# Performance work log

Hardware: AMD Instinct MI355X
Metric: run time of the kernel (lower is better)

## Reference

```python
import jax, jax.numpy as jnp
import numpy as np

N, E = 2048, 32768
IN_ND, ND = 128, 256
IN_ED, ED = 64, 128
OUT_D = 256
H, FF, NL = 8, 1024, 3
MAX_DEG = 64
L = 5


def setup_inputs() -> dict:
    key = jax.random.key(0)
    ks = jax.random.split(key, 20)
    s = 0.02
    return dict(
        x=jax.random.normal(ks[0], (N, IN_ND), jnp.float32),
        edge_index=jax.random.randint(ks[1], (2, E), 0, N),
        edge_attr=jax.random.normal(ks[2], (E, IN_ED), jnp.float32),
        node_dist=jax.random.randint(ks[3], (N, N), 0, 7, dtype=jnp.int32),
        edge_paths=jax.random.randint(ks[4], (N, N, L), 0, E, dtype=jnp.int32),
        Wn_in=jax.random.normal(ks[5], (IN_ND, ND)) * s,
        bn_in=jnp.zeros((ND,)),
        We_in=jax.random.normal(ks[6], (IN_ED, ED)) * s,
        be_in=jnp.zeros((ED,)),
        z_in=jax.random.normal(ks[7], (MAX_DEG, ND)) * s,
        z_out=jax.random.normal(ks[8], (MAX_DEG, ND)) * s,
        b_spatial=jax.random.normal(ks[9], (L,)) * s,
        ln1_w=jnp.ones((NL, ND)), ln1_b=jnp.zeros((NL, ND)),
        ln2_w=jnp.ones((NL, ND)), ln2_b=jnp.zeros((NL, ND)),
        Wq=jax.random.normal(ks[10], (NL, H, ND, ND)) * s,
        bq=jnp.zeros((NL, H, ND)),
        Wk=jax.random.normal(ks[11], (NL, H, ND, ND)) * s,
        bk=jnp.zeros((NL, H, ND)),
        Wv=jax.random.normal(ks[12], (NL, H, ND, ND)) * s,
        bv=jnp.zeros((NL, H, ND)),
        edge_vec=jax.random.normal(ks[13], (NL, H, L, ED)) * s,
        Wo=jax.random.normal(ks[14], (NL, H * ND, ND)) * s,
        bo=jnp.zeros((NL, ND)),
        Wff1=jax.random.normal(ks[15], (NL, ND, FF)) * s,
        bff1=jnp.zeros((NL, FF)),
        Wff2=jax.random.normal(ks[16], (NL, FF, ND)) * s,
        bff2=jnp.zeros((NL, ND)),
        Wout=jax.random.normal(ks[17], (ND, OUT_D)) * s,
        bout=jnp.zeros((OUT_D,)),
    )


def _ln(x, w, b, eps=1e-5):
    m = x.mean(-1, keepdims=True)
    v = ((x - m) ** 2).mean(-1, keepdims=True)
    return (x - m) * jax.lax.rsqrt(v + eps) * w + b


def _forward(x, edge_attr, Wn_in, bn_in, We_in, be_in, z_in, z_out, b_spatial,
             ln1_w, ln1_b, ln2_w, ln2_b, Wq, bq, Wk, bk, Wv, bv, edge_vec,
             Wo, bo, Wff1, bff1, Wff2, bff2, Wout, bout,
             edge_index, node_dist, edge_paths):
    n = x.shape[0]
    h = x @ Wn_in + bn_in                      # node_in_lin
    e = edge_attr @ We_in + be_in              # edge_in_lin
    # centrality encoding: degree embeddings, clipped to table size - 1
    in_deg = jnp.zeros((n,), jnp.int32).at[edge_index[1]].add(1)
    out_deg = jnp.zeros((n,), jnp.int32).at[edge_index[0]].add(1)
    h = h + z_in[jnp.clip(in_deg, 0, z_in.shape[0] - 1)] \
          + z_out[jnp.clip(out_deg, 0, z_out.shape[0] - 1)]
    # spatial encoding: b[min(path_len, L) - 1], 0 where unreachable
    Lmax = b_spatial.shape[0]
    b_mat = jnp.where(node_dist > 0,
                      b_spatial[jnp.clip(node_dist, 1, Lmax) - 1],
                      jnp.zeros((), h.dtype))          # [N,N]
    n_pe = jnp.clip(node_dist - 1, 0, Lmax)            # edges on path
    inv_len = jnp.where(n_pe > 0,
                        1.0 / jnp.maximum(n_pe, 1).astype(h.dtype),
                        jnp.zeros((), h.dtype))        # [N,N]
    nl, nh, _, dk = Wq.shape
    scale = 1.0 / jnp.sqrt(jnp.asarray(dk, h.dtype))
    for l in range(nl):
        xn = _ln(h, ln1_w[l], ln1_b[l])
        q = jnp.einsum('nd,hdk->hnk', xn, Wq[l]) + bq[l][:, None, :]
        k = jnp.einsum('nd,hdk->hnk', xn, Wk[l]) + bk[l][:, None, :]
        v = jnp.einsum('nd,hdk->hnk', xn, Wv[l]) + bv[l][:, None, :]
        # edge encoding: per-head dot of edge_vector[step] with each edge feature,
        # then gather along the stored shortest path and mean over its length
        dots = jnp.einsum('hld,ed->hle', edge_vec[l], e)   # [H,L,E]
        c = jnp.zeros((nh, n, n), h.dtype)
        for s in range(Lmax):  # fixed small loop over path steps
            d_s = jnp.take(dots[:, s, :], edge_paths[:, :, s], axis=1)  # [H,N,N]
            valid = (s < n_pe)[None]                                    # [1,N,N]
            c = c + jnp.where(valid, d_s, jnp.zeros((), h.dtype))
        c = c * inv_len[None]
        a = jnp.einsum('hnk,hmk->hnm', q, k) * scale + b_mat[None] + c
        attn = jax.nn.softmax(a, axis=-1)
        o = jnp.einsum('hnm,hmk->hnk', attn, v)            # [H,N,dk]
        o = jnp.transpose(o, (1, 0, 2)).reshape(n, nh * dk)
        h = o @ Wo[l] + bo[l] + h                          # attn + residual
        x2 = _ln(h, ln2_w[l], ln2_b[l])
        h = jax.nn.gelu(x2 @ Wff1[l] + bff1[l], approximate=False) @ Wff2[l] + bff2[l] + h
    return h @ Wout + bout


def reference(x, edge_index, edge_attr, node_dist, edge_paths,
              Wn_in, bn_in, We_in, be_in, z_in, z_out, b_spatial,
              ln1_w, ln1_b, ln2_w, ln2_b, Wq, bq, Wk, bk, Wv, bv, edge_vec,
              Wo, bo, Wff1, bff1, Wff2, bff2, Wout, bout):
    return _forward(x, edge_attr, Wn_in, bn_in, We_in, be_in, z_in, z_out,
                    b_spatial, ln1_w, ln1_b, ln2_w, ln2_b, Wq, bq, Wk, bk,
                    Wv, bv, edge_vec, Wo, bo, Wff1, bff1, Wff2, bff2,
                    Wout, bout, edge_index, node_dist, edge_paths)
```

## Files before the change

kernel.cpp:

```cpp
#include <hip/hip_runtime.h>


constexpr int NN    = 2048;
constexpr int EE    = 32768;
constexpr int IN_ND = 128;
constexpr int ND    = 256;
constexpr int IN_ED = 64;
constexpr int ED    = 128;
constexpr int H     = 8;
constexpr int FF    = 1024;
constexpr int NL    = 3;
constexpr int LMAX  = 5;
constexpr int MAXDEG= 64;
constexpr int SPLIT = 4;
constexpr int KSP   = NN / SPLIT;
constexpr int QROWS = 256;

enum { E_NONE = 0, E_BIAS = 1, E_BIAS_RES = 2, E_BIAS_GELU = 3 };

using u16 = unsigned short;
using short8 = __attribute__((ext_vector_type(8))) short;
using f32x4  = __attribute__((ext_vector_type(4))) float;
using u32x4  = __attribute__((ext_vector_type(4))) unsigned int;

__device__ __forceinline__ u16 f2bf(float f) {
    unsigned u = __float_as_uint(f);
    u += 0x7fff + ((u >> 16) & 1);
    return (u16)(u >> 16);
}
__device__ __forceinline__ float bf2f(u16 h) {
    return __uint_as_float((unsigned)h << 16);
}
__device__ __forceinline__ float gelu_f(float x) {
    return 0.5f * x * (1.0f + erff(x * 0.70710678118654752440f));
}

#define GLL16(gsrc, ldst)                                                     \
    __builtin_amdgcn_global_load_lds(                                         \
        (const __attribute__((address_space(1))) void*)(gsrc),                \
        (__attribute__((address_space(3))) void*)(ldst), 16, 0, 0)

template<int EPI, int OBF>
__global__ __launch_bounds__(256)
void mgemm_k(const u16* __restrict__ A, int lda, long aZs,
             const u16* __restrict__ B, int ldb, long bZs,
             void* __restrict__ Cp, int ldc, long cZs,
             int K, const float* __restrict__ bias0,
             const float* __restrict__ bias1, const float* __restrict__ bias2)
{
    const int z = blockIdx.z;
    A += (long)z * aZs;
    B += (long)z * bZs;
    const float* bias = (z == 0) ? bias0 : (z == 1 ? bias1 : bias2);
    const int row0 = blockIdx.y * 128, col0 = blockIdx.x * 128;
    const int tid = threadIdx.x;
    const int lane = tid & 63, wv = tid >> 6;
    const int wr = wv >> 1, wc = wv & 1;
    const int fl = lane & 15, kg = lane >> 4;

    __shared__ u16 As[128 * 32];
    __shared__ u16 Bs[128 * 32];

    int aoff[4], boff[4];
#pragma unroll
    for (int m = 0; m < 4; m++) {
        int r = wr * 64 + m * 16 + fl;
        aoff[m] = r * 64 + ((kg ^ ((r >> 1) & 3)) * 16);
        r = wc * 64 + m * 16 + fl;
        boff[m] = r * 64 + ((kg ^ ((r >> 1) & 3)) * 16);
    }

    const int id0 = tid * 2, id1 = id0 + 1;
    const int sr0 = id0 >> 2, sl0 = id0 & 3;
    const int sr1 = id1 >> 2, sl1 = id1 & 3;
    const int wb0 = sr0 * 64 + ((sl0 ^ ((sr0 >> 1) & 3)) * 16);
    const int wb1 = sr1 * 64 + ((sl1 ^ ((sr1 >> 1) & 3)) * 16);
    const u16* ga0 = A + (long)(row0 + sr0) * lda + sl0 * 8;
    const u16* ga1 = A + (long)(row0 + sr1) * lda + sl1 * 8;
    const u16* gb0 = B + (long)(col0 + sr0) * ldb + sl0 * 8;
    const u16* gb1 = B + (long)(col0 + sr1) * ldb + sl1 * 8;

    const f32x4 zero = {0.f, 0.f, 0.f, 0.f};
    f32x4 acc[4][4];
#pragma unroll
    for (int m = 0; m < 4; m++)
#pragma unroll
        for (int n = 0; n < 4; n++) acc[m][n] = zero;

    for (int k0 = 0; k0 < K; k0 += 32) {
        const uint4 va0 = *(const uint4*)(ga0 + k0);
        const uint4 va1 = *(const uint4*)(ga1 + k0);
        const uint4 vb0 = *(const uint4*)(gb0 + k0);
        const uint4 vb1 = *(const uint4*)(gb1 + k0);
        __syncthreads();
        *(uint4*)((char*)As + wb0) = va0;
        *(uint4*)((char*)As + wb1) = va1;
        *(uint4*)((char*)Bs + wb0) = vb0;
        *(uint4*)((char*)Bs + wb1) = vb1;
        __syncthreads();
        short8 af[4], bfr[4];
#pragma unroll
        for (int m = 0; m < 4; m++)
            af[m] = *(const short8*)((const char*)As + aoff[m]);
#pragma unroll
        for (int n = 0; n < 4; n++)
            bfr[n] = *(const short8*)((const char*)Bs + boff[n]);
#pragma unroll
        for (int m = 0; m < 4; m++)
#pragma unroll
            for (int n = 0; n < 4; n++)
                acc[m][n] = __builtin_amdgcn_mfma_f32_16x16x32_bf16(
                    af[m], bfr[n], acc[m][n], 0, 0, 0);
    }

    float* Cf = (float*)Cp + (long)z * cZs;
    u16*   Cb = (u16*)Cp   + (long)z * cZs;
#pragma unroll
    for (int n = 0; n < 4; n++) {
        const int col = col0 + wc * 64 + n * 16 + fl;
        float bcol = 0.f;
        if constexpr (EPI == E_BIAS || EPI == E_BIAS_RES || EPI == E_BIAS_GELU)
            bcol = bias[col];
#pragma unroll
        for (int m = 0; m < 4; m++) {
            const f32x4 v = acc[m][n];
#pragma unroll
            for (int r = 0; r < 4; r++) {
                const int row = row0 + wr * 64 + m * 16 + kg * 4 + r;
                float x = v[r];
                if constexpr (EPI == E_BIAS)       x += bcol;
                else if constexpr (EPI == E_BIAS_RES)  x += bcol + Cf[(long)row * ldc + col];
                else if constexpr (EPI == E_BIAS_GELU) x = gelu_f(x + bcol);
                if constexpr (OBF) Cb[(long)row * ldc + col] = f2bf(x);
                else               Cf[(long)row * ldc + col] = x;
            }
        }
    }
}

template<int EPI, int OBF>
__global__ __launch_bounds__(256)
void mgemm64_k(const u16* __restrict__ A, int lda,
               const u16* __restrict__ B, int ldb,
               void* __restrict__ Cp, int ldc,
               int K, const float* __restrict__ bias)
{
    const int row0 = blockIdx.y * 64, col0 = blockIdx.x * 64;
    const int tid = threadIdx.x, lane = tid & 63, w = tid >> 6;
    const int wr = w >> 1, wc = w & 1;
    const int fl = lane & 15, kg = lane >> 4;

    __shared__ u16 As[64 * 64];
    __shared__ u16 Bs[64 * 64];

    int aoff[2][2], boff[2][2];
#pragma unroll
    for (int m = 0; m < 2; m++)
#pragma unroll
        for (int ks = 0; ks < 2; ks++) {
            int r = wr * 32 + m * 16 + fl;
            aoff[m][ks] = r * 64 + (((ks * 4 + kg) ^ (r & 7)) * 8);
            r = wc * 32 + m * 16 + fl;
            boff[m][ks] = r * 64 + (((ks * 4 + kg) ^ (r & 7)) * 8);
        }
    const int i0 = tid, i1 = tid + 256;
    const int ar0 = i0 >> 3, as0 = i0 & 7, ar1 = i1 >> 3, as1 = i1 & 7;
    const u16* gA0 = A + (long)(row0 + ar0) * lda + ((as0 ^ (ar0 & 7)) * 8);
    const u16* gA1 = A + (long)(row0 + ar1) * lda + ((as1 ^ (ar1 & 7)) * 8);
    const u16* gB0 = B + (long)(col0 + ar0) * ldb + ((as0 ^ (ar0 & 7)) * 8);
    const u16* gB1 = B + (long)(col0 + ar1) * ldb + ((as1 ^ (ar1 & 7)) * 8);

    const f32x4 zero = {0.f, 0.f, 0.f, 0.f};
    f32x4 acc[2][2];
#pragma unroll
    for (int m = 0; m < 2; m++)
#pragma unroll
        for (int n = 0; n < 2; n++) acc[m][n] = zero;

    for (int k0 = 0; k0 < K; k0 += 64) {
        const uint4 a0 = *(const uint4*)(gA0 + k0);
        const uint4 a1 = *(const uint4*)(gA1 + k0);
        const uint4 b0 = *(const uint4*)(gB0 + k0);
        const uint4 b1 = *(const uint4*)(gB1 + k0);
        __syncthreads();
        *(uint4*)((char*)As + i0 * 16) = a0;
        *(uint4*)((char*)As + i1 * 16) = a1;
        *(uint4*)((char*)Bs + i0 * 16) = b0;
        *(uint4*)((char*)Bs + i1 * 16) = b1;
        __syncthreads();
        short8 af[2][2], bf_[2][2];
#pragma unroll
        for (int m = 0; m < 2; m++)
#pragma unroll
            for (int ks = 0; ks < 2; ks++) {
                af[m][ks]  = *(const short8*)(As + aoff[m][ks]);
                bf_[m][ks] = *(const short8*)(Bs + boff[m][ks]);
            }
#pragma unroll
        for (int m = 0; m < 2; m++)
#pragma unroll
            for (int n = 0; n < 2; n++)
#pragma unroll
                for (int ks = 0; ks < 2; ks++)
                    acc[m][n] = __builtin_amdgcn_mfma_f32_16x16x32_bf16(
                        af[m][ks], bf_[n][ks], acc[m][n], 0, 0, 0);
    }

    float* Cf = (float*)Cp;
    u16*   Cb = (u16*)Cp;
#pragma unroll
    for (int n = 0; n < 2; n++) {
        const int col = col0 + wc * 32 + n * 16 + fl;
        float bcol = 0.f;
        if constexpr (EPI == E_BIAS || EPI == E_BIAS_RES || EPI == E_BIAS_GELU)
            bcol = bias[col];
#pragma unroll
        for (int m = 0; m < 2; m++) {
            const f32x4 v = acc[m][n];
#pragma unroll
            for (int r = 0; r < 4; r++) {
                const int row = row0 + wr * 32 + m * 16 + kg * 4 + r;
                float x = v[r];
                if constexpr (EPI == E_BIAS)       x += bcol;
                else if constexpr (EPI == E_BIAS_RES)  x += bcol + Cf[(long)row * ldc + col];
                else if constexpr (EPI == E_BIAS_GELU) x = gelu_f(x + bcol);
                if constexpr (OBF) Cb[(long)row * ldc + col] = f2bf(x);
                else               Cf[(long)row * ldc + col] = x;
            }
        }
    }
}

__global__ __launch_bounds__(1024, 4)
void fattn_k(const u16* __restrict__ qb, const u16* __restrict__ kb,
             const u16* __restrict__ vT, u16* __restrict__ sc,
             float* __restrict__ ml)
{
    const int hh = blockIdx.x;
    const int row0 = blockIdx.y * QROWS;
    const int sp = blockIdx.z;
    const int kbase = sp * KSP;
    constexpr int NT = KSP / 32;
    const int tid = threadIdx.x, lane = tid & 63, w = tid >> 6;
    const int fl = lane & 15, kg = lane >> 4;
    const long NN2 = (long)NN * NN;

    __shared__ u16 Ks[3 * 32 * 256];
    __shared__ u16 Vs[3 * 256 * 32];
    __shared__ u16 Bls[2 * 256 * 32];
    __shared__ u16 Ps[16 * 16 * 40];

    auto stage = [&](int t, int buf) {
        const int kt0 = kbase + t * 32;
        const int kr = tid >> 5, ksl = tid & 31;
        GLL16(kb + (long)(kt0 + kr) * (H * ND) + hh * ND + ((ksl ^ (kr & 7)) * 8),
              Ks + buf * 8192 + tid * 8);
        const int vr = tid >> 2, vsl = tid & 3;
        GLL16(vT + (long)(hh * ND + vr) * NN + kt0 + ((vsl ^ ((vr >> 1) & 3)) * 8),
              Vs + buf * 8192 + tid * 8);
    };
    auto stage_bias = [&](int t, int buf) {
        const u16* g = sc + (long)hh * NN2 + (long)(row0 + (tid >> 2)) * NN
                     + kbase + t * 32 + (tid & 3) * 8;
        GLL16(g, Bls + buf * 8192 + tid * 8);
    };

    short8 qf[8];
    {
        const u16* qrow = qb + (long)(row0 + w * 16 + fl) * (H * ND) + hh * ND;
#pragma unroll
        for (int ks = 0; ks < 8; ks++)
            qf[ks] = *(const short8*)(qrow + ks * 32 + kg * 8);
    }
    stage_bias(0, 0);
    stage(0, 0);
    stage(1, 1);

    short8 ones;
#pragma unroll
    for (int i = 0; i < 8; i++) ones[i] = (short)0x3F80;

    f32x4 O[16];
#pragma unroll
    for (int of = 0; of < 16; of++) O[of] = f32x4{0.f, 0.f, 0.f, 0.f};
    f32x4 lac = {0.f, 0.f, 0.f, 0.f};

    const float scale = 1.f / 16.f;
    for (int t = 0; t < NT; t++) {
        asm volatile("s_waitcnt vmcnt(2)" ::: "memory");
        __builtin_amdgcn_sched_barrier(0);
        asm volatile("s_barrier" ::: "memory");
        __builtin_amdgcn_sched_barrier(0);

        stage_bias((t + 1) % NT, (t + 1) & 1);
        stage((t + 2) % NT, (t + 2) % 3);

        const int cb = t % 3;
        f32x4 s[2] = {f32x4{0.f,0.f,0.f,0.f}, f32x4{0.f,0.f,0.f,0.f}};
        __builtin_amdgcn_s_setprio(1);
#pragma unroll
        for (int ks = 0; ks < 8; ks++)
#pragma unroll
            for (int cf = 0; cf < 2; cf++) {
                const int mlr = cf * 16 + fl;
                const short8 kf = *(const short8*)(Ks + cb * 8192 + mlr * 256
                                                   + (((ks * 4 + kg) ^ (mlr & 7)) * 8));
                s[cf] = __builtin_amdgcn_mfma_f32_16x16x32_bf16(qf[ks], kf, s[cf], 0, 0, 0);
            }
        __builtin_amdgcn_s_setprio(0);

        const u16* bl = Bls + (t & 1) * 8192 + (w * 16 + kg * 4) * 32;
        float p[2][4];
#pragma unroll
        for (int cf = 0; cf < 2; cf++)
#pragma unroll
            for (int r = 0; r < 4; r++)
                p[cf][r] = __expf(s[cf][r] * scale
                                  + bf2f(bl[r * 32 + cf * 16 + fl]));
#pragma unroll
        for (int cf = 0; cf < 2; cf++)
#pragma unroll
            for (int r = 0; r < 4; r++)
                Ps[w * 640 + (kg * 4 + r) * 40 + cf * 16 + fl] = f2bf(p[cf][r]);

        const short8 pa = *(const short8*)(Ps + w * 640 + fl * 40 + kg * 8);
        __builtin_amdgcn_s_setprio(1);
        lac = __builtin_amdgcn_mfma_f32_16x16x32_bf16(pa, ones, lac, 0, 0, 0);
#pragma unroll
        for (int of = 0; of < 16; of++) {
            const int d = of * 16 + fl;
            const short8 vf = *(const short8*)(Vs + cb * 8192 + d * 32
                                               + ((kg ^ ((d >> 1) & 3)) * 8));
            O[of] = __builtin_amdgcn_mfma_f32_16x16x32_bf16(pa, vf, O[of], 0, 0, 0);
        }
        __builtin_amdgcn_s_setprio(0);
    }

    u16* op = sc + (long)hh * NN2 + sp * KSP;
#pragma unroll
    for (int of = 0; of < 16; of++)
#pragma unroll
        for (int r = 0; r < 4; r++) {
            const int row = row0 + w * 16 + kg * 4 + r;
            op[(long)row * NN + of * 16 + fl] = f2bf(O[of][r]);
        }
    if (fl == 0) {
#pragma unroll
        for (int r = 0; r < 4; r++) {
            const int row = row0 + w * 16 + kg * 4 + r;
            ml[((long)sp * H + hh) * NN + row] = lac[r];
        }
    }
}

__global__ __launch_bounds__(256)
void combine_k(const u16* __restrict__ sc, const float* __restrict__ ml,
               u16* __restrict__ o2)
{
    const int idx = blockIdx.x * 256 + threadIdx.x;
    const int d8 = idx & 31;
    const int n  = (idx >> 5) & (NN - 1);
    const int h  = idx >> 16;
    const long NN2 = (long)NN * NN;
    float L = 0.f;
#pragma unroll
    for (int z = 0; z < SPLIT; z++)
        L += ml[((long)z * H + h) * NN + n];
    const float invL = 1.f / L;
    float acc[8] = {0.f,0.f,0.f,0.f,0.f,0.f,0.f,0.f};
#pragma unroll
    for (int z = 0; z < SPLIT; z++) {
        const u32x4 q = *(const u32x4*)(sc + (long)h * NN2 + (long)n * NN
                                        + z * KSP + d8 * 8);
        acc[0] += bf2f(q.x & 0xffff); acc[1] += bf2f(q.x >> 16);
        acc[2] += bf2f(q.y & 0xffff); acc[3] += bf2f(q.y >> 16);
        acc[4] += bf2f(q.z & 0xffff); acc[5] += bf2f(q.z >> 16);
        acc[6] += bf2f(q.w & 0xffff); acc[7] += bf2f(q.w >> 16);
    }
    uint4 o;
    o.x = (unsigned)f2bf(acc[0] * invL) | ((unsigned)f2bf(acc[1] * invL) << 16);
    o.y = (unsigned)f2bf(acc[2] * invL) | ((unsigned)f2bf(acc[3] * invL) << 16);
    o.z = (unsigned)f2bf(acc[4] * invL) | ((unsigned)f2bf(acc[5] * invL) << 16);
    o.w = (unsigned)f2bf(acc[6] * invL) | ((unsigned)f2bf(acc[7] * invL) << 16);
    *(uint4*)(o2 + (long)n * (H * ND) + h * ND + d8 * 8) = o;
}

template<int INF32>
__global__ __launch_bounds__(256)
void transp_k(const void* __restrict__ inp, long inZs,
              u16* __restrict__ out, long outZs, int R, int C)
{
    const int z = blockIdx.z;
    const int r0 = blockIdx.y * 64, c0 = blockIdx.x * 64;
    __shared__ u16 t[64][68];
    const int tx = threadIdx.x & 63, ty = threadIdx.x >> 6;
    if constexpr (INF32) {
        const float* in = (const float*)inp + (long)z * inZs;
#pragma unroll
        for (int i = 0; i < 16; i++) {
            const int r = i * 4 + ty;
            t[r][tx] = f2bf(in[(long)(r0 + r) * C + c0 + tx]);
        }
    } else {
        const u16* in = (const u16*)inp + (long)z * inZs;
#pragma unroll
        for (int i = 0; i < 16; i++) {
            const int r = i * 4 + ty;
            t[r][tx] = in[(long)(r0 + r) * C + c0 + tx];
        }
    }
    __syncthreads();
    u16* o = out + (long)z * outZs;
#pragma unroll
    for (int i = 0; i < 16; i++) {
        const int r = i * 4 + ty;
        o[(long)(c0 + r) * R + r0 + tx] = t[tx][r];
    }
}

__global__ __launch_bounds__(256)
void cvt_k(const float* __restrict__ in, u16* __restrict__ out)
{
    const long i = (long)blockIdx.x * 256 + threadIdx.x;
    const float4 v = ((const float4*)in)[i];
    ushort4 o;
    o.x = f2bf(v.x); o.y = f2bf(v.y); o.z = f2bf(v.z); o.w = f2bf(v.w);
    ((ushort4*)out)[i] = o;
}

__global__ __launch_bounds__(256)
void ln_k(const float* __restrict__ x, const float* __restrict__ w,
          const float* __restrict__ b, u16* __restrict__ y)
{
    const int wid = threadIdx.x >> 6, lane = threadIdx.x & 63;
    const int row = blockIdx.x * 4 + wid;
    const float4 v = reinterpret_cast<const float4*>(x + (long)row * ND)[lane];
    float s = v.x + v.y + v.z + v.w;
#pragma unroll
    for (int o = 32; o >= 1; o >>= 1) s += __shfl_xor(s, o);
    const float mean = s * (1.f / ND);
    const float d0 = v.x - mean, d1 = v.y - mean, d2 = v.z - mean, d3 = v.w - mean;
    float sq = d0 * d0 + d1 * d1 + d2 * d2 + d3 * d3;
#pragma unroll
    for (int o = 32; o >= 1; o >>= 1) sq += __shfl_xor(sq, o);
    const float rstd = rsqrtf(sq * (1.f / ND) + 1e-5f);
    const float4 wv = reinterpret_cast<const float4*>(w)[lane];
    const float4 bv = reinterpret_cast<const float4*>(b)[lane];
    ushort4 o4;
    o4.x = f2bf(d0 * rstd * wv.x + bv.x);
    o4.y = f2bf(d1 * rstd * wv.y + bv.y);
    o4.z = f2bf(d2 * rstd * wv.z + bv.z);
    o4.w = f2bf(d3 * rstd * wv.w + bv.w);
    reinterpret_cast<ushort4*>(y + (long)row * ND)[lane] = o4;
}

__global__ __launch_bounds__(256)
void dotsT_k(const u16* __restrict__ e, const float* __restrict__ evl,
             u16* __restrict__ dtb)
{
    const int s = blockIdx.y;
    const int ei = blockIdx.x * 256 + threadIdx.x;
    __shared__ float evs[H * ED];
    for (int i = threadIdx.x; i < H * ED; i += 256)
        evs[i] = evl[((i >> 7) * LMAX + s) * ED + (i & 127)];
    __syncthreads();
    const uint4* er = (const uint4*)(e + (long)ei * ED);
    float c[H];
#pragma unroll
    for (int h = 0; h < H; h++) c[h] = 0.f;
#pragma unroll
    for (int d8 = 0; d8 < ED / 8; d8++) {
        const uint4 q = er[d8];
        float f[8];
        f[0] = bf2f(q.x & 0xffff); f[1] = bf2f(q.x >> 16);
        f[2] = bf2f(q.y & 0xffff); f[3] = bf2f(q.y >> 16);
        f[4] = bf2f(q.z & 0xffff); f[5] = bf2f(q.z >> 16);
        f[6] = bf2f(q.w & 0xffff); f[7] = bf2f(q.w >> 16);
#pragma unroll
        for (int h = 0; h < H; h++) {
            const float* w = &evs[h * ED + d8 * 8];
            c[h] += w[0] * f[0] + w[1] * f[1] + w[2] * f[2] + w[3] * f[3]
                  + w[4] * f[4] + w[5] * f[5] + w[6] * f[6] + w[7] * f[7];
        }
    }
    uint4 o;
    o.x = (unsigned)f2bf(c[0]) | ((unsigned)f2bf(c[1]) << 16);
    o.y = (unsigned)f2bf(c[2]) | ((unsigned)f2bf(c[3]) << 16);
    o.z = (unsigned)f2bf(c[4]) | ((unsigned)f2bf(c[5]) << 16);
    o.w = (unsigned)f2bf(c[6]) | ((unsigned)f2bf(c[7]) << 16);
    *(uint4*)(dtb + ((long)s * EE + ei) * H) = o;
}

__global__ __launch_bounds__(256)
void pack_k(const int* __restrict__ ndist, const int* __restrict__ epaths,
            unsigned* __restrict__ pc0, unsigned* __restrict__ pc1,
            unsigned* __restrict__ pc2)
{
    const long idx = (long)blockIdx.x * 256 + threadIdx.x;
    const unsigned d = (unsigned)ndist[idx];
    const int* ep = epaths + idx * LMAX;
    const unsigned e0 = ep[0], e1 = ep[1], e2 = ep[2], e3 = ep[3], e4 = ep[4];
    pc0[idx] = d | (e0 << 8);
    pc1[idx] = e1 | (e2 << 16);
    pc2[idx] = e3 | (e4 << 16);
}

__global__ __launch_bounds__(256)
void bias_k(const unsigned* __restrict__ pc0, const unsigned* __restrict__ pc1,
            const unsigned* __restrict__ pc2, const float* __restrict__ bspat,
            const u16* __restrict__ dtb, u16* __restrict__ sc)
{
    const long idx = (long)blockIdx.x * 256 + threadIdx.x;
    const unsigned w0 = pc0[idx], w1 = pc1[idx], w2 = pc2[idx];
    const int d = (int)(w0 & 255u);
    float bb = 0.f;
    if (d > 0) bb = bspat[(d < LMAX ? d : LMAX) - 1];
    int npe = d - 1;
    npe = npe < 0 ? 0 : (npe > LMAX ? LMAX : npe);
    const int ep[LMAX] = { (int)(w0 >> 8), (int)(w1 & 0xffffu), (int)(w1 >> 16),
                           (int)(w2 & 0xffffu), (int)(w2 >> 16) };
    float c[H];
#pragma unroll
    for (int h = 0; h < H; h++) c[h] = 0.f;
#pragma unroll
    for (int s = 0; s < LMAX; s++) {
        if (s < npe) {
            const uint4 q = *(const uint4*)(dtb + ((long)s * EE + ep[s]) * H);
            c[0] += bf2f(q.x & 0xffff); c[1] += bf2f(q.x >> 16);
            c[2] += bf2f(q.y & 0xffff); c[3] += bf2f(q.y >> 16);
            c[4] += bf2f(q.z & 0xffff); c[5] += bf2f(q.z >> 16);
            c[6] += bf2f(q.w & 0xffff); c[7] += bf2f(q.w >> 16);
        }
    }
    const float inv = npe > 0 ? 1.f / (float)npe : 0.f;
    const long NN2 = (long)NN * NN;
#pragma unroll
    for (int h = 0; h < H; h++)
        sc[(long)h * NN2 + idx] = f2bf(bb + c[h] * inv);
}

__global__ void deg_k(const int* __restrict__ ei, int* __restrict__ ind,
                      int* __restrict__ outd)
{
    const int e = blockIdx.x * 256 + threadIdx.x;
    atomicAdd(&outd[ei[e]], 1);
    atomicAdd(&ind[ei[EE + e]], 1);
}

__global__ void degembed_k(float* __restrict__ h, const int* __restrict__ ind,
                           const int* __restrict__ outd,
                           const float* __restrict__ z_in,
                           const float* __restrict__ z_out)
{
    const int idx = blockIdx.x * 256 + threadIdx.x;
    const int n = idx >> 8, c = idx & 255;
    int di = ind[n];  di = di > (MAXDEG - 1) ? (MAXDEG - 1) : di;
    int dw = outd[n]; dw = dw > (MAXDEG - 1) ? (MAXDEG - 1) : dw;
    h[idx] += z_in[di * ND + c] + z_out[dw * ND + c];
}

__global__ void sentinel_k(float* o) { o[0] = 12345.0f; }

extern "C" void kernel_launch(void* const* d_in, const int* in_sizes, int n_in,
                              void* d_out, int out_size, void* d_ws, size_t ws_size,
                              hipStream_t stream)
{
    const float* x      = (const float*)d_in[0];
    const int*   eidx   = (const int*)d_in[1];
    const float* eattr  = (const float*)d_in[2];
    const int*   ndist  = (const int*)d_in[3];
    const int*   epaths = (const int*)d_in[4];
    const float* Wn_in  = (const float*)d_in[5];
    const float* bn_in  = (const float*)d_in[6];
    const float* We_in  = (const float*)d_in[7];
    const float* be_in  = (const float*)d_in[8];
    const float* z_in   = (const float*)d_in[9];
    const float* z_out  = (const float*)d_in[10];
    const float* bspat  = (const float*)d_in[11];
    const float* ln1w   = (const float*)d_in[12];
    const float* ln1b   = (const float*)d_in[13];
    const float* ln2w   = (const float*)d_in[14];
    const float* ln2b   = (const float*)d_in[15];
    const float* Wq     = (const float*)d_in[16];
    const float* bq     = (const float*)d_in[17];
    const float* Wk     = (const float*)d_in[18];
    const float* bk     = (const float*)d_in[19];
    const float* Wv     = (const float*)d_in[20];
    const float* bv     = (const float*)d_in[21];
    const float* evec   = (const float*)d_in[22];
    const float* Wo     = (const float*)d_in[23];
    const float* bo     = (const float*)d_in[24];
    const float* Wff1   = (const float*)d_in[25];
    const float* bff1   = (const float*)d_in[26];
    const float* Wff2   = (const float*)d_in[27];
    const float* bff2   = (const float*)d_in[28];
    const float* Wout   = (const float*)d_in[29];
    const float* bout   = (const float*)d_in[30];
    float* out = (float*)d_out;

    char* p = (char*)d_ws;
    auto alloc = [&](size_t bytes) -> char* {
        char* r = p;
        p += (bytes + 255) & ~(size_t)255;
        return r;
    };
    float* h    = (float*)alloc((size_t)NN * ND * 4);
    u16*   hb   = (u16*)alloc((size_t)NN * ND * 2);
    u16*   xb   = (u16*)alloc((size_t)NN * IN_ND * 2);
    u16*   xnb  = (u16*)alloc((size_t)NN * ND * 2);
    u16*   eb   = (u16*)alloc((size_t)EE * IN_ED * 2);
    u16*   e_bf = (u16*)alloc((size_t)EE * ED * 2);
    u16*   qb   = (u16*)alloc((size_t)NN * H * ND * 2);
    u16*   kb   = (u16*)alloc((size_t)NN * H * ND * 2);
    u16*   vb   = (u16*)alloc((size_t)NN * H * ND * 2);
    u16*   vT   = (u16*)alloc((size_t)NN * H * ND * 2);
    u16*   o2   = (u16*)alloc((size_t)NN * H * ND * 2);
    u16*   ff1b = (u16*)alloc((size_t)NN * FF * 2);
    u16*   dtb  = (u16*)alloc((size_t)LMAX * EE * H * 2);
    u16*   WqT  = (u16*)alloc((size_t)NL * H * ND * ND * 2);
    u16*   WkT  = (u16*)alloc((size_t)NL * H * ND * ND * 2);
    u16*   WvT  = (u16*)alloc((size_t)NL * H * ND * ND * 2);
    u16*   WoT  = (u16*)alloc((size_t)NL * ND * H * ND * 2);
    u16*   W1T  = (u16*)alloc((size_t)NL * FF * ND * 2);
    u16*   W2T  = (u16*)alloc((size_t)NL * ND * FF * 2);
    u16*   WnT  = (u16*)alloc((size_t)ND * IN_ND * 2);
    u16*   WeT  = (u16*)alloc((size_t)ED * IN_ED * 2);
    u16*   WouT = (u16*)alloc((size_t)ND * ND * 2);
    int*   ind  = (int*)alloc(NN * 4);
    int*   outd = (int*)alloc(NN * 4);
    unsigned* pc0 = (unsigned*)alloc((size_t)NN * NN * 4);
    unsigned* pc1 = (unsigned*)alloc((size_t)NN * NN * 4);
    unsigned* pc2 = (unsigned*)alloc((size_t)NN * NN * 4);
    float* ml   = (float*)alloc((size_t)SPLIT * H * NN * 4);
    u16*   sc   = (u16*)alloc((size_t)H * NN * NN * 2);
    if ((size_t)(p - (char*)d_ws) > ws_size) {
        sentinel_k<<<1, 1, 0, stream>>>(out);
        return;
    }

    const long NN2 = (long)NN * NN;

    hipMemsetAsync(ind, 0, NN * 4, stream);
    hipMemsetAsync(outd, 0, NN * 4, stream);
    deg_k<<<EE / 256, 256, 0, stream>>>(eidx, ind, outd);
    pack_k<<<(int)(NN2 / 256), 256, 0, stream>>>(ndist, epaths, pc0, pc1, pc2);

    cvt_k<<<NN * IN_ND / 1024, 256, 0, stream>>>(x, xb);
    cvt_k<<<EE * IN_ED / 1024, 256, 0, stream>>>(eattr, eb);
    transp_k<1><<<dim3(4, 4, NL * H), 256, 0, stream>>>(Wq, ND * ND, WqT, ND * ND, ND, ND);
    transp_k<1><<<dim3(4, 4, NL * H), 256, 0, stream>>>(Wk, ND * ND, WkT, ND * ND, ND, ND);
    transp_k<1><<<dim3(4, 4, NL * H), 256, 0, stream>>>(Wv, ND * ND, WvT, ND * ND, ND, ND);
    transp_k<1><<<dim3(4, 32, NL), 256, 0, stream>>>(Wo, (long)H * ND * ND, WoT, (long)H * ND * ND, H * ND, ND);
    transp_k<1><<<dim3(16, 4, NL), 256, 0, stream>>>(Wff1, (long)ND * FF, W1T, (long)ND * FF, ND, FF);
    transp_k<1><<<dim3(4, 16, NL), 256, 0, stream>>>(Wff2, (long)ND * FF, W2T, (long)ND * FF, FF, ND);
    transp_k<1><<<dim3(4, 2, 1), 256, 0, stream>>>(Wn_in, 0, WnT, 0, IN_ND, ND);
    transp_k<1><<<dim3(2, 1, 1), 256, 0, stream>>>(We_in, 0, WeT, 0, IN_ED, ED);
    transp_k<1><<<dim3(4, 4, 1), 256, 0, stream>>>(Wout, 0, WouT, 0, ND, ND);

    mgemm64_k<E_BIAS, 0><<<dim3(4, 32), 256, 0, stream>>>(
        xb, IN_ND, WnT, IN_ND, h, ND, IN_ND, bn_in);
    degembed_k<<<NN * ND / 256, 256, 0, stream>>>(h, ind, outd, z_in, z_out);
    mgemm64_k<E_BIAS, 1><<<dim3(2, EE / 64), 256, 0, stream>>>(
        eb, IN_ED, WeT, IN_ED, e_bf, ED, IN_ED, be_in);

    for (int l = 0; l < NL; l++) {
        ln_k<<<NN / 4, 256, 0, stream>>>(h, ln1w + l * ND, ln1b + l * ND, xnb);

        mgemm_k<E_BIAS, 1><<<dim3(16, 16, 3), 256, 0, stream>>>(
            xnb, ND, 0,
            WqT + (size_t)l * H * ND * ND, ND, (long)NL * H * ND * ND,
            qb, H * ND, (long)NN * H * ND,
            ND, bq + l * H * ND, bk + l * H * ND, bv + l * H * ND);
        transp_k<0><<<dim3(32, 32, 1), 256, 0, stream>>>(vb, 0, vT, 0, NN, H * ND);

        dotsT_k<<<dim3(EE / 256, LMAX), 256, 0, stream>>>(
            e_bf, evec + (size_t)l * H * LMAX * ED, dtb);
        bias_k<<<(int)(NN2 / 256), 256, 0, stream>>>(pc0, pc1, pc2, bspat, dtb, sc);

        fattn_k<<<dim3(H, NN / QROWS, SPLIT), 1024, 0, stream>>>(qb, kb, vT, sc, ml);
        combine_k<<<H * NN * 32 / 256, 256, 0, stream>>>(sc, ml, o2);

        mgemm64_k<E_BIAS_RES, 0><<<dim3(4, 32), 256, 0, stream>>>(
            o2, H * ND, WoT + (size_t)l * ND * H * ND, H * ND, h, ND, H * ND, bo + l * ND);

        ln_k<<<NN / 4, 256, 0, stream>>>(h, ln2w + l * ND, ln2b + l * ND, xnb);
        mgemm64_k<E_BIAS_GELU, 1><<<dim3(16, 32), 256, 0, stream>>>(
            xnb, ND, W1T + (size_t)l * FF * ND, ND, ff1b, FF, ND, bff1 + l * FF);
        mgemm64_k<E_BIAS_RES, 0><<<dim3(4, 32), 256, 0, stream>>>(
            ff1b, FF, W2T + (size_t)l * ND * FF, FF, h, ND, FF, bff2 + l * ND);
    }

    cvt_k<<<NN * ND / 1024, 256, 0, stream>>>(h, hb);
    mgemm64_k<E_BIAS, 0><<<dim3(4, 32), 256, 0, stream>>>(
        hb, ND, WouT, ND, out, ND, ND, bout);
}
```

Measured before the change: 741.3 us.

## Split attention into smaller blocks and replace triple-buffered staging with single buffer

The fused attention kernel now runs 512-thread blocks over 128 query rows and splits the key range 8 ways instead of 4, which quadruples the grid. The triple-buffered K/V and double-buffered bias staging in shared memory is replaced by a single buffer, refilled after a barrier at the end of each iteration. The goal is to free LDS and raise the number of resident blocks per CU, so other blocks hide memory latency instead of in-block prefetch. The cost is losing the software pipelining inside a block, paying an extra barrier and a full vmcnt(0) wait per tile, and producing more partial results for the combine step.

```diff
diff --git a/kernel.cpp b/kernel.cpp
--- a/kernel.cpp
+++ b/kernel.cpp
@@ -12,9 +12,9 @@
 constexpr int NL    = 3;
 constexpr int LMAX  = 5;
 constexpr int MAXDEG= 64;
-constexpr int SPLIT = 4;
+constexpr int SPLIT = 8;
 constexpr int KSP   = NN / SPLIT;
-constexpr int QROWS = 256;
+constexpr int QROWS = 128;
 
 enum { E_NONE = 0, E_BIAS = 1, E_BIAS_RES = 2, E_BIAS_GELU = 3 };
 
@@ -231,7 +231,7 @@
     }
 }
 
-__global__ __launch_bounds__(1024, 4)
+__global__ __launch_bounds__(512, 4)
 void fattn_k(const u16* __restrict__ qb, const u16* __restrict__ kb,
              const u16* __restrict__ vT, u16* __restrict__ sc,
              float* __restrict__ ml)
@@ -245,24 +245,28 @@
     const int fl = lane & 15, kg = lane >> 4;
     const long NN2 = (long)NN * NN;
 
-    __shared__ u16 Ks[3 * 32 * 256];
-    __shared__ u16 Vs[3 * 256 * 32];
-    __shared__ u16 Bls[2 * 256 * 32];
-    __shared__ u16 Ps[16 * 16 * 40];
-
-    auto stage = [&](int t, int buf) {
+    __shared__ u16 Ks[32 * 256];
+    __shared__ u16 Vs[256 * 32];
+    __shared__ u16 Bls[QROWS * 32];
+    __shared__ u16 Ps[8 * 16 * 40];
+
+    auto stage = [&](int t) {
         const int kt0 = kbase + t * 32;
-        const int kr = tid >> 5, ksl = tid & 31;
-        GLL16(kb + (long)(kt0 + kr) * (H * ND) + hh * ND + ((ksl ^ (kr & 7)) * 8),
-              Ks + buf * 8192 + tid * 8);
-        const int vr = tid >> 2, vsl = tid & 3;
-        GLL16(vT + (long)(hh * ND + vr) * NN + kt0 + ((vsl ^ ((vr >> 1) & 3)) * 8),
-              Vs + buf * 8192 + tid * 8);
+#pragma unroll
+        for (int c = 0; c < 2; c++) {
+            const int idx = c * 512 + tid;
+            const int kr = idx >> 5, ksl = idx & 31;
+            GLL16(kb + (long)(kt0 + kr) * (H * ND) + hh * ND + ((ksl ^ (kr & 7)) * 8),
+                  Ks + idx * 8);
+            const int vr = idx >> 2, vsl = idx & 3;
+            GLL16(vT + (long)(hh * ND + vr) * NN + kt0 + ((vsl ^ ((vr >> 1) & 3)) * 8),
+                  Vs + idx * 8);
+        }
     };
-    auto stage_bias = [&](int t, int buf) {
+    auto stage_bias = [&](int t) {
         const u16* g = sc + (long)hh * NN2 + (long)(row0 + (tid >> 2)) * NN
                      + kbase + t * 32 + (tid & 3) * 8;
-        GLL16(g, Bls + buf * 8192 + tid * 8);
+        GLL16(g, Bls + tid * 8);
     };
 
     short8 qf[8];
@@ -272,9 +276,8 @@
         for (int ks = 0; ks < 8; ks++)
             qf[ks] = *(const short8*)(qrow + ks * 32 + kg * 8);
     }
-    stage_bias(0, 0);
-    stage(0, 0);
-    stage(1, 1);
+    stage(0);
+    stage_bias(0);
 
     short8 ones;
 #pragma unroll
@@ -287,15 +290,11 @@
 
     const float scale = 1.f / 16.f;
     for (int t = 0; t < NT; t++) {
-        asm volatile("s_waitcnt vmcnt(2)" ::: "memory");
+        asm volatile("s_waitcnt vmcnt(0)" ::: "memory");
         __builtin_amdgcn_sched_barrier(0);
         asm volatile("s_barrier" ::: "memory");
         __builtin_amdgcn_sched_barrier(0);
 
-        stage_bias((t + 1) % NT, (t + 1) & 1);
-        stage((t + 2) % NT, (t + 2) % 3);
-
-        const int cb = t % 3;
         f32x4 s[2] = {f32x4{0.f,0.f,0.f,0.f}, f32x4{0.f,0.f,0.f,0.f}};
         __builtin_amdgcn_s_setprio(1);
 #pragma unroll
@@ -303,13 +302,13 @@
 #pragma unroll
             for (int cf = 0; cf < 2; cf++) {
                 const int mlr = cf * 16 + fl;
-                const short8 kf = *(const short8*)(Ks + cb * 8192 + mlr * 256
+                const short8 kf = *(const short8*)(Ks + mlr * 256
                                                    + (((ks * 4 + kg) ^ (mlr & 7)) * 8));
                 s[cf] = __builtin_amdgcn_mfma_f32_16x16x32_bf16(qf[ks], kf, s[cf], 0, 0, 0);
             }
         __builtin_amdgcn_s_setprio(0);
 
-        const u16* bl = Bls + (t & 1) * 8192 + (w * 16 + kg * 4) * 32;
+        const u16* bl = Bls + (w * 16 + kg * 4) * 32;
         float p[2][4];
 #pragma unroll
         for (int cf = 0; cf < 2; cf++)
@@ -329,11 +328,20 @@
 #pragma unroll
         for (int of = 0; of < 16; of++) {
             const int d = of * 16 + fl;
-            const short8 vf = *(const short8*)(Vs + cb * 8192 + d * 32
+            const short8 vf = *(const short8*)(Vs + d * 32
                                                + ((kg ^ ((d >> 1) & 3)) * 8));
             O[of] = __builtin_amdgcn_mfma_f32_16x16x32_bf16(pa, vf, O[of], 0, 0, 0);
         }
         __builtin_amdgcn_s_setprio(0);
+
+        asm volatile("s_waitcnt lgkmcnt(0)" ::: "memory");
+        __builtin_amdgcn_sched_barrier(0);
+        asm volatile("s_barrier" ::: "memory");
+        __builtin_amdgcn_sched_barrier(0);
+        if (t + 1 < NT) {
+            stage(t + 1);
+            stage_bias(t + 1);
+        }
     }
 
     u16* op = sc + (long)hh * NN2 + sp * KSP;
@@ -677,7 +685,7 @@
             e_bf, evec + (size_t)l * H * LMAX * ED, dtb);
         bias_k<<<(int)(NN2 / 256), 256, 0, stream>>>(pc0, pc1, pc2, bspat, dtb, sc);
 
-        fattn_k<<<dim3(H, NN / QROWS, SPLIT), 1024, 0, stream>>>(qb, kb, vT, sc, ml);
+        fattn_k<<<dim3(H, NN / QROWS, SPLIT), 512, 0, stream>>>(qb, kb, vT, sc, ml);
         combine_k<<<H * NN * 32 / 256, 256, 0, stream>>>(sc, ml, o2);
 
         mgemm64_k<E_BIAS_RES, 0><<<dim3(4, 32), 256, 0, stream>>>(
```

After: 1.234 ms. +66.4%, slower.
